# Kernel tuning notes

Hardware: AMD Instinct MI355X
Metric: run time of the kernel (lower is better)

Reference implementation:

```python
import jax, jax.numpy as jnp
import numpy as np

H = 4  # num_heads


def setup_inputs() -> dict:
    key = jax.random.key(0)
    ks = jax.random.split(key, 9)
    B, N, Cin, Chid = 4, 2048, 256, 256
    Cs = Cin // 4
    f = lambda k, shape: jax.random.normal(k, shape, dtype=jnp.float32)
    return {
        "s": f(ks[0], (B, N, Cin)),
        "h": f(ks[1], (B, N, Cs)),
        "sh": f(ks[2], (B, N, Chid)),
        "temperature": jnp.ones((H, 1, 1), jnp.float32) * 0.1,
        "temperature2": jnp.ones((H, 1, 1), jnp.float32) * 0.1,
        "Wq_c": f(ks[3], (Cin, Cin)) * 0.02,
        "Wq_s": f(ks[4], (Chid, Chid)) * 0.02,
        "Wk_c": f(ks[5], (Chid, Chid)) * 0.02,
        "Wv_c": f(ks[6], (Chid, Chid)) * 0.02,
        "Wk_s": f(ks[7], (Chid, Chid)) * 0.02,
        "Wv_s": f(ks[8], (Cs, Cs)) * 0.02,
    }


def reference(s, h, sh, temperature, temperature2, Wq_c, Wq_s, Wk_c, Wv_c, Wk_s, Wv_s):
    B, N, C = sh.shape
    C_c = s.shape[2]
    C_s = h.shape[2]
    d = C // H
    d_c = C_c // H
    d_s = C_s // H

    # projections (Linear without bias: x @ W.T)
    q_c = (s @ Wq_c.T).reshape(B, H, N, d_c).swapaxes(-1, -2)  # (B,H,d_c,N)
    q_s = (sh @ Wq_s.T).reshape(B, H, N, d)
    k_c = (sh @ Wk_c.T).reshape(B, H, N, d)
    v_c = (sh @ Wv_c.T).reshape(B, H, N, d)
    k_s = (sh @ Wk_s.T).reshape(B, H, N, d)
    v_s = (h @ Wv_s.T).reshape(B, H, N, d_s)

    scale = 1.0 / jnp.sqrt(jnp.float32(d))

    # channel branch: (B,H,d_c,N)@(B,H,N,d) -> (B,H,d_c,d)
    attn_ca = jax.nn.softmax((q_c @ k_c) * scale * temperature, axis=-1)
    # dropout is identity at inference
    x_ca = (attn_ca @ v_c.swapaxes(-2, -1)).reshape(B, N, C_c)  # raw reshape, faithful to torch

    # spatial branch: (B,H,N,N)
    attn_sa = jax.nn.softmax(
        jnp.einsum("bhnd,bhmd->bhnm", q_s, k_s) * scale * temperature2, axis=-1
    )
    x_sa = (attn_sa @ v_s).reshape(B, N, C_s)  # raw reshape, faithful to torch

    return jnp.concatenate([x_ca, x_sa], axis=2)  # (B,N,C_c+C_s)
```

## Files before the change

### kernel.cpp

```cpp
#include <hip/hip_runtime.h>
#include <math.h>


constexpr int Bb = 4, Nn = 2048, Hh = 4;
constexpr int PROJ_EL = Nn * 256;
constexpr int HEAD_EL = Nn * 64;

typedef __attribute__((ext_vector_type(8))) short short8_t;
typedef __attribute__((ext_vector_type(4))) float f32x4;

__device__ __forceinline__ ushort f2bf(float x) {
    union { float f; unsigned u; } v; v.f = x;
    unsigned r = v.u + 0x7fffu + ((v.u >> 16) & 1u);
    return (ushort)(r >> 16);
}
__device__ __forceinline__ float bf2f(ushort x) {
    union { unsigned u; float f; } v; v.u = ((unsigned)x) << 16;
    return v.f;
}
__device__ __forceinline__ void gl_lds16(const ushort* g, ushort* l) {
    __builtin_amdgcn_global_load_lds(
        (const __attribute__((address_space(1))) void*)g,
        (__attribute__((address_space(3))) void*)l, 16, 0, 0);
}

constexpr size_t OFF_SB    = 0;
constexpr size_t OFF_SHB   = OFF_SB   + 1024 * 1024;
constexpr size_t OFF_HB    = OFF_SHB  + 1024 * 1024;
constexpr size_t OFF_WQC   = OFF_HB   + 256 * 1024;
constexpr size_t OFF_WCAT  = OFF_WQC  + 32 * 1024;
constexpr size_t OFF_PQC   = OFF_WCAT + 128 * 1024;
constexpr size_t OFF_PQS   = OFF_PQC  + 1024 * 1024;
constexpr size_t OFF_PKC   = OFF_PQS  + 1024 * 1024;
constexpr size_t OFF_PVC   = OFF_PKC  + 1024 * 1024;
constexpr size_t OFF_PKS   = OFF_PVC  + 1024 * 1024;
constexpr size_t OFF_PVST  = OFF_PKS  + 1024 * 1024;
constexpr size_t OFF_PART  = OFF_PVST + 256 * 1024;
constexpr size_t OFF_SCA   = OFF_PART + 512 * 1024;
constexpr size_t OFF_WVS   = OFF_SCA  + 32 * 1024;

constexpr unsigned SEG0 = 2097152;
constexpr unsigned SEG1 = SEG0 + 2097152;
constexpr unsigned SEG2 = SEG1 + 524288;
constexpr unsigned SEG3 = SEG2 + 65536;
constexpr unsigned SEG4 = SEG3 + 65536;
constexpr unsigned SEG5 = SEG4 + 65536;
constexpr unsigned SEG6 = SEG5 + 65536;
constexpr unsigned SEG7 = SEG6 + 65536;
constexpr unsigned SEG8 = SEG7 + 4096;

__global__ __launch_bounds__(256) void convert_all(
    const float* __restrict__ s, const float* __restrict__ sh,
    const float* __restrict__ h, const float* __restrict__ wqc,
    const float* __restrict__ wqs, const float* __restrict__ wkc,
    const float* __restrict__ wvc, const float* __restrict__ wks,
    const float* __restrict__ wvs,
    ushort* __restrict__ sb, ushort* __restrict__ shb, ushort* __restrict__ hb,
    ushort* __restrict__ wqcb, ushort* __restrict__ wcatb, ushort* __restrict__ wvsb)
{
    unsigned e = (blockIdx.x * 256u + threadIdx.x) * 8u;
    if (e >= SEG8) return;
    const float* src; ushort* dst; unsigned off;
    if      (e < SEG0) { src = s;   dst = sb;             off = e; }
    else if (e < SEG1) { src = sh;  dst = shb;            off = e - SEG0; }
    else if (e < SEG2) { src = h;   dst = hb;             off = e - SEG1; }
    else if (e < SEG3) { src = wqc; dst = wqcb;           off = e - SEG2; }
    else if (e < SEG4) { src = wqs; dst = wcatb;          off = e - SEG3; }
    else if (e < SEG5) { src = wkc; dst = wcatb + 65536;  off = e - SEG4; }
    else if (e < SEG6) { src = wvc; dst = wcatb + 131072; off = e - SEG5; }
    else if (e < SEG7) { src = wks; dst = wcatb + 196608; off = e - SEG6; }
    else               { src = wvs; dst = wvsb;           off = e - SEG7; }
    float4 f0 = *(const float4*)&src[off];
    float4 f1 = *(const float4*)&src[off + 4];
    short8_t o;
    o[0] = f2bf(f0.x); o[1] = f2bf(f0.y); o[2] = f2bf(f0.z); o[3] = f2bf(f0.w);
    o[4] = f2bf(f1.x); o[5] = f2bf(f1.y); o[6] = f2bf(f1.z); o[7] = f2bf(f1.w);
    *(short8_t*)&dst[off] = o;
}

__device__ __forceinline__ void gemm_tile_body(
    const ushort* __restrict__ X, const ushort* __restrict__ W,
    ushort* __restrict__ d0, ushort* __restrict__ d1,
    ushort* __restrict__ d2, ushort* __restrict__ d3, int K,
    int m0, int n0, ushort (*Xs)[64], ushort (*Ws)[64])
{
    const int t = threadIdx.x;
    const int w = t >> 6, l = t & 63, c = l & 15, g = l >> 4;
    const int wr = w >> 1, wc = w & 1;
    const int r8 = l >> 3;

    f32x4 acc[4][4] = {};

    for (int k0 = 0; k0 < K; k0 += 64) {
        __syncthreads();
        #pragma unroll
        for (int q = 0; q < 4; ++q) {
            const int rbase = w * 32 + q * 8;
            const int row = rbase + r8;
            const int slot = (l & 7) ^ (row & 7);
            gl_lds16(&X[(size_t)(m0 + row) * K + k0 + slot * 8], &Xs[rbase][0]);
            gl_lds16(&W[(size_t)(n0 + row) * K + k0 + slot * 8], &Ws[rbase][0]);
        }
        __syncthreads();
        #pragma unroll
        for (int ks = 0; ks < 2; ++ks) {
            short8_t af[4], bf[4];
            #pragma unroll
            for (int rt = 0; rt < 4; ++rt) {
                const int R = wr * 64 + rt * 16 + c;
                af[rt] = *(const short8_t*)&Xs[R][(((4 * ks + g) ^ (R & 7)) * 8)];
            }
            #pragma unroll
            for (int ct = 0; ct < 4; ++ct) {
                const int R = wc * 64 + ct * 16 + c;
                bf[ct] = *(const short8_t*)&Ws[R][(((4 * ks + g) ^ (R & 7)) * 8)];
            }
            #pragma unroll
            for (int rt = 0; rt < 4; ++rt)
                #pragma unroll
                for (int ct = 0; ct < 4; ++ct)
                    acc[rt][ct] = __builtin_amdgcn_mfma_f32_16x16x32_bf16(
                        af[rt], bf[ct], acc[rt][ct], 0, 0, 0);
        }
    }

    const int seg = n0 >> 8;
    ushort* dst = seg == 0 ? d0 : seg == 1 ? d1 : seg == 2 ? d2 : d3;
    const int colbase = (n0 & 255) + wc * 64;
    #pragma unroll
    for (int rt = 0; rt < 4; ++rt)
        #pragma unroll
        for (int ct = 0; ct < 4; ++ct)
            #pragma unroll
            for (int r = 0; r < 4; ++r) {
                int mrow = m0 + wr * 64 + rt * 16 + 4 * g + r;
                int col = colbase + ct * 16 + c;
                dst[(size_t)mrow * 256 + col] = f2bf(acc[rt][ct][r]);
            }
}

__device__ __forceinline__ void vs_tile_body(
    const ushort* __restrict__ Wvs, const ushort* __restrict__ Hb,
    ushort* __restrict__ Cvt, int vbid)
{
    const int t = threadIdx.x;
    const int w = t >> 6, l = t & 63, c = l & 15, g = l >> 4;
    const int n0 = vbid * 256 + w * 64;

    f32x4 acc[4][4] = {};
    #pragma unroll
    for (int ks = 0; ks < 2; ++ks) {
        short8_t af[4], bfr[4];
        #pragma unroll
        for (int rt = 0; rt < 4; ++rt)
            af[rt] = *(const short8_t*)&Wvs[(size_t)(rt * 16 + c) * 64 + ks * 32 + 8 * g];
        #pragma unroll
        for (int ct = 0; ct < 4; ++ct)
            bfr[ct] = *(const short8_t*)&Hb[(size_t)(n0 + ct * 16 + c) * 64 + ks * 32 + 8 * g];
        #pragma unroll
        for (int rt = 0; rt < 4; ++rt)
            #pragma unroll
            for (int ct = 0; ct < 4; ++ct)
                acc[rt][ct] = __builtin_amdgcn_mfma_f32_16x16x32_bf16(
                    af[rt], bfr[ct], acc[rt][ct], 0, 0, 0);
    }
    #pragma unroll
    for (int rt = 0; rt < 4; ++rt)
        #pragma unroll
        for (int ct = 0; ct < 4; ++ct)
            #pragma unroll
            for (int r = 0; r < 4; ++r) {
                int cc = rt * 16 + 4 * g + r;
                int m  = n0 + ct * 16 + c;
                int b  = m >> 11, n = m & 2047;
                int L  = n * 64 + cc;
                int hh = L >> 15;
                int k  = (L & 32767) >> 4;
                int d  = L & 15;
                Cvt[(size_t)((b * 4 + hh) * 16 + d) * 2048 + k] = f2bf(acc[rt][ct][r]);
            }
}

__global__ __launch_bounds__(256) void proj_all(
    const ushort* __restrict__ shb, const ushort* __restrict__ wcatb,
    ushort* __restrict__ Pqs, ushort* __restrict__ Pkc,
    ushort* __restrict__ Pvc, ushort* __restrict__ Pks,
    const ushort* __restrict__ sb, const ushort* __restrict__ wqcb,
    ushort* __restrict__ Pqc,
    const ushort* __restrict__ wvsb, const ushort* __restrict__ hb,
    ushort* __restrict__ PvsT)
{
    __shared__ ushort Xs[128][64];
    __shared__ ushort Ws[128][64];
    const int bid = blockIdx.x;
    if (bid < 512) {
        gemm_tile_body(shb, wcatb, Pqs, Pkc, Pvc, Pks, 256,
                       (bid >> 3) * 128, (bid & 7) * 128, Xs, Ws);
    } else if (bid < 640) {
        const int r = bid - 512;
        gemm_tile_body(sb, wqcb, Pqc, Pqc, Pqc, Pqc, 256,
                       (r >> 1) * 128, (r & 1) * 128, Xs, Ws);
    } else {
        vs_tile_body(wvsb, hb, PvsT, bid - 640);
    }
}

__global__ __launch_bounds__(256) void chan_qk_mfma(const ushort* __restrict__ Pqc,
                                                    const ushort* __restrict__ Pkc,
                                                    float* __restrict__ part)
{
    const int ch = blockIdx.x, hh = blockIdx.y, b = blockIdx.z;
    const ushort* Q = Pqc + (size_t)b * PROJ_EL + (size_t)hh * HEAD_EL;
    const ushort* Kk = Pkc + (size_t)b * PROJ_EL + (size_t)hh * HEAD_EL;
    __shared__ ushort Qt[64][72];
    __shared__ ushort Kt[64][72];
    const int t = threadIdx.x;
    const int w = t >> 6, l = t & 63, c = l & 15, g = l >> 4;
    const int srow = t & 63;
    const int scol0 = (t >> 6) * 8;

    f32x4 acc[4] = {};

    for (int sub = 0; sub < 4; ++sub) {
        const int r0 = ch * 256 + sub * 64;
        __syncthreads();
        #pragma unroll
        for (int pass = 0; pass < 2; ++pass) {
            const int cbase = scol0 + pass * 32;
            short8_t qv = *(const short8_t*)&Q[(size_t)(r0 + srow) * 64 + cbase];
            short8_t kv = *(const short8_t*)&Kk[(size_t)(r0 + srow) * 64 + cbase];
            #pragma unroll
            for (int j = 0; j < 8; ++j) {
                Qt[cbase + j][srow] = (ushort)qv[j];
                Kt[cbase + j][srow] = (ushort)kv[j];
            }
        }
        __syncthreads();
        #pragma unroll
        for (int ks = 0; ks < 2; ++ks) {
            short8_t af = *(const short8_t*)&Qt[w * 16 + c][ks * 32 + 8 * g];
            #pragma unroll
            for (int ct = 0; ct < 4; ++ct) {
                short8_t bf = *(const short8_t*)&Kt[ct * 16 + c][ks * 32 + 8 * g];
                acc[ct] = __builtin_amdgcn_mfma_f32_16x16x32_bf16(af, bf, acc[ct], 0, 0, 0);
            }
        }
    }

    float* P = part + (((size_t)(b * 4 + hh) * 8 + ch) << 12);
    #pragma unroll
    for (int ct = 0; ct < 4; ++ct)
        #pragma unroll
        for (int r = 0; r < 4; ++r)
            P[(w * 16 + 4 * g + r) * 64 + ct * 16 + c] = acc[ct][r];
}

__global__ __launch_bounds__(256) void chan_softmax(const float* __restrict__ part,
                                                    const float* __restrict__ temp,
                                                    ushort* __restrict__ Sca)
{
    const int bh = blockIdx.x;
    const int hsel = bh & 3;
    const int t = threadIdx.x;
    const int i = t >> 2, q = t & 3;
    const float sT = 0.125f * temp[hsel];

    float v[16];
    #pragma unroll
    for (int jj = 0; jj < 16; ++jj) v[jj] = 0.f;
    #pragma unroll
    for (int cc = 0; cc < 8; ++cc) {
        const float* p = &part[((size_t)bh * 8 + cc) * 4096 + i * 64 + q * 16];
        #pragma unroll
        for (int j4 = 0; j4 < 4; ++j4) {
            float4 f = *(const float4*)&p[j4 * 4];
            v[j4 * 4 + 0] += f.x; v[j4 * 4 + 1] += f.y;
            v[j4 * 4 + 2] += f.z; v[j4 * 4 + 3] += f.w;
        }
    }
    float m = -1e30f;
    #pragma unroll
    for (int jj = 0; jj < 16; ++jj) { v[jj] *= sT; m = fmaxf(m, v[jj]); }
    m = fmaxf(m, __shfl_xor(m, 1, 4));
    m = fmaxf(m, __shfl_xor(m, 2, 4));
    float sum = 0.f;
    #pragma unroll
    for (int jj = 0; jj < 16; ++jj) { v[jj] = __expf(v[jj] - m); sum += v[jj]; }
    sum += __shfl_xor(sum, 1, 4);
    sum += __shfl_xor(sum, 2, 4);
    const float inv = 1.0f / sum;
    ushort* dst = &Sca[((size_t)bh << 12) + i * 64 + q * 16];
    #pragma unroll
    for (int j4 = 0; j4 < 4; ++j4) {
        ushort4 r;
        r.x = f2bf(v[j4 * 4 + 0] * inv); r.y = f2bf(v[j4 * 4 + 1] * inv);
        r.z = f2bf(v[j4 * 4 + 2] * inv); r.w = f2bf(v[j4 * 4 + 3] * inv);
        *(ushort4*)&dst[j4 * 4] = r;
    }
}

__device__ __forceinline__ void chan_pv_body(
    const ushort* __restrict__ Sca, const ushort* __restrict__ Pvc,
    float* __restrict__ out, int b, int hh, int nc, int wv, int l)
{
    const int c = l & 15, g = l >> 4;
    const ushort* S = Sca + ((size_t)(b * 4 + hh) << 12);
    const ushort* V = Pvc + (size_t)b * PROJ_EL + (size_t)hh * HEAD_EL;
    const int n0w = nc * 256 + wv * 64;

    f32x4 acc[4][4] = {};
    #pragma unroll
    for (int ks = 0; ks < 2; ++ks) {
        short8_t af[4], bfr[4];
        #pragma unroll
        for (int rt = 0; rt < 4; ++rt)
            af[rt] = *(const short8_t*)&S[(size_t)(rt * 16 + c) * 64 + ks * 32 + 8 * g];
        #pragma unroll
        for (int ct = 0; ct < 4; ++ct)
            bfr[ct] = *(const short8_t*)&V[(size_t)(n0w + ct * 16 + c) * 64 + ks * 32 + 8 * g];
        #pragma unroll
        for (int rt = 0; rt < 4; ++rt)
            #pragma unroll
            for (int ct = 0; ct < 4; ++ct)
                acc[rt][ct] = __builtin_amdgcn_mfma_f32_16x16x32_bf16(
                    af[rt], bfr[ct], acc[rt][ct], 0, 0, 0);
    }

    float* ob = out + (size_t)b * (Nn * 320);
    #pragma unroll
    for (int rt = 0; rt < 4; ++rt)
        #pragma unroll
        for (int ct = 0; ct < 4; ++ct)
            #pragma unroll
            for (int r = 0; r < 4; ++r) {
                int i = rt * 16 + 4 * g + r;
                int nn = n0w + ct * 16 + c;
                int rem = hh * 131072 + i * 2048 + nn;
                ob[(rem >> 8) * 320 + (rem & 255)] = acc[rt][ct][r];
            }
}

__global__ __launch_bounds__(512, 2) void spatial_pv(
    const ushort* __restrict__ Pqs, const ushort* __restrict__ Pks,
    const ushort* __restrict__ PvsT, const float* __restrict__ temp2,
    const ushort* __restrict__ Sca, const ushort* __restrict__ Pvc,
    float* __restrict__ out)
{
    if (blockIdx.x < 64) {
        const int task = blockIdx.x * 8 + (threadIdx.x >> 6);
        const int b2 = task >> 7, rem = task & 127;
        const int hh2 = rem >> 5, rem2 = rem & 31;
        const int nc = rem2 >> 2, wv = rem2 & 3;
        chan_pv_body(Sca, Pvc, out, b2, hh2, nc, wv, threadIdx.x & 63);
        return;
    }

    const int i0 = blockIdx.x - 64;
    const int xcd = i0 & 7, j = i0 >> 3;
    const int hsel = xcd + 8 * (j & 1);
    const int qb = j >> 1;
    const int b = hsel >> 2, hh = hsel & 3;

    const int t = threadIdx.x, w = t >> 6, l = t & 63;
    const int c = l & 15, g = l >> 4;
    const int qg = w >> 1, kh = w & 1;

    __shared__ ushort Kbuf[2][2][64][72];
    __shared__ ushort Vbuf[2][2][16][72];
    __shared__ ushort P_lds[8][2][16][72];
    __shared__ float  O_red[8][2][16][16];
    __shared__ float  L_red[8][2][16];

    const ushort* Qh = Pqs + (size_t)b * PROJ_EL + (size_t)hh * HEAD_EL;
    const ushort* Kh = Pks + (size_t)b * PROJ_EL + (size_t)hh * HEAD_EL;
    const ushort* Vt = PvsT + (size_t)((b * 4 + hh) * 16) * 2048;
    const float sT2 = 0.125f * temp2[hh] * 1.44269504f;

    const int q0 = qb * 128 + qg * 32;
    const ushort* qpA = Qh + (size_t)(q0 + c) * 64 + 8 * g;
    const ushort* qpB = qpA + 16 * 64;
    const short8_t qfA0 = *(const short8_t*)qpA;
    const short8_t qfA1 = *(const short8_t*)(qpA + 32);
    const short8_t qfB0 = *(const short8_t*)qpB;
    const short8_t qfB1 = *(const short8_t*)(qpB + 32);

    f32x4 oaccA = {0.f, 0.f, 0.f, 0.f}, oaccB = {0.f, 0.f, 0.f, 0.f};
    float lsumA = 0.f, lsumB = 0.f;
    ushort* PwA = &P_lds[w][0][0][0];
    ushort* PwB = &P_lds[w][1][0][0];

    const int sh_ = t >> 8, th = t & 255;
    const int krow = th >> 2, ksub = (th & 3) * 16;
    const int vrow = th >> 4, vcol = (th & 15) * 4;

    {
        const int kb = (sh_ * 16) * 64;
        short8_t k0 = *(const short8_t*)&Kh[(size_t)(kb + krow) * 64 + ksub];
        short8_t k1 = *(const short8_t*)&Kh[(size_t)(kb + krow) * 64 + ksub + 8];
        uint2 v0 = *(const uint2*)&Vt[(size_t)vrow * 2048 + kb + vcol];
        *(short8_t*)&Kbuf[sh_][0][krow][ksub]     = k0;
        *(short8_t*)&Kbuf[sh_][0][krow][ksub + 8] = k1;
        *(uint2*)&Vbuf[sh_][0][vrow][vcol] = v0;
    }

    short8_t kreg0, kreg1; uint2 vreg;
    for (int it = 0; it < 16; ++it) {
        const int cur = it & 1;

        if (it < 15) {
            const int nb = (sh_ * 16 + it + 1) * 64;
            kreg0 = *(const short8_t*)&Kh[(size_t)(nb + krow) * 64 + ksub];
            kreg1 = *(const short8_t*)&Kh[(size_t)(nb + krow) * 64 + ksub + 8];
            vreg = *(const uint2*)&Vt[(size_t)vrow * 2048 + nb + vcol];
        }

        __syncthreads();

        #pragma unroll
        for (int tc = 0; tc < 4; ++tc) {
            short8_t kf0 = *(const short8_t*)&Kbuf[kh][cur][tc * 16 + c][8 * g];
            short8_t kf1 = *(const short8_t*)&Kbuf[kh][cur][tc * 16 + c][32 + 8 * g];
            f32x4 z = {0.f, 0.f, 0.f, 0.f};
            f32x4 sa = __builtin_amdgcn_mfma_f32_16x16x32_bf16(kf0, qfA0, z, 0, 0, 0);
            sa = __builtin_amdgcn_mfma_f32_16x16x32_bf16(kf1, qfA1, sa, 0, 0, 0);
            f32x4 sb2 = __builtin_amdgcn_mfma_f32_16x16x32_bf16(kf0, qfB0, z, 0, 0, 0);
            sb2 = __builtin_amdgcn_mfma_f32_16x16x32_bf16(kf1, qfB1, sb2, 0, 0, 0);

            float a0 = __builtin_amdgcn_exp2f(sa[0] * sT2);
            float a1 = __builtin_amdgcn_exp2f(sa[1] * sT2);
            float a2 = __builtin_amdgcn_exp2f(sa[2] * sT2);
            float a3 = __builtin_amdgcn_exp2f(sa[3] * sT2);
            lsumA += (a0 + a1) + (a2 + a3);
            unsigned ua, ub;
            asm("v_cvt_pk_bf16_f32 %0, %1, %2" : "=v"(ua) : "v"(a0), "v"(a1));
            asm("v_cvt_pk_bf16_f32 %0, %1, %2" : "=v"(ub) : "v"(a2), "v"(a3));
            *(unsigned*)&PwA[(size_t)c * 72 + tc * 16 + 4 * g]     = ua;
            *(unsigned*)&PwA[(size_t)c * 72 + tc * 16 + 4 * g + 2] = ub;

            float b0 = __builtin_amdgcn_exp2f(sb2[0] * sT2);
            float b1 = __builtin_amdgcn_exp2f(sb2[1] * sT2);
            float b2 = __builtin_amdgcn_exp2f(sb2[2] * sT2);
            float b3 = __builtin_amdgcn_exp2f(sb2[3] * sT2);
            lsumB += (b0 + b1) + (b2 + b3);
            unsigned vb0, vb1;
            asm("v_cvt_pk_bf16_f32 %0, %1, %2" : "=v"(vb0) : "v"(b0), "v"(b1));
            asm("v_cvt_pk_bf16_f32 %0, %1, %2" : "=v"(vb1) : "v"(b2), "v"(b3));
            *(unsigned*)&PwB[(size_t)c * 72 + tc * 16 + 4 * g]     = vb0;
            *(unsigned*)&PwB[(size_t)c * 72 + tc * 16 + 4 * g + 2] = vb1;
        }
        __builtin_amdgcn_sched_barrier(0);
        #pragma unroll
        for (int ks = 0; ks < 2; ++ks) {
            short8_t vf = *(const short8_t*)&Vbuf[kh][cur][c][ks * 32 + 8 * g];
            short8_t pfA = *(const short8_t*)&PwA[(size_t)c * 72 + ks * 32 + 8 * g];
            oaccA = __builtin_amdgcn_mfma_f32_16x16x32_bf16(vf, pfA, oaccA, 0, 0, 0);
            short8_t pfB = *(const short8_t*)&PwB[(size_t)c * 72 + ks * 32 + 8 * g];
            oaccB = __builtin_amdgcn_mfma_f32_16x16x32_bf16(vf, pfB, oaccB, 0, 0, 0);
        }

        if (it < 15) {
            *(short8_t*)&Kbuf[sh_][cur ^ 1][krow][ksub]     = kreg0;
            *(short8_t*)&Kbuf[sh_][cur ^ 1][krow][ksub + 8] = kreg1;
            *(uint2*)&Vbuf[sh_][cur ^ 1][vrow][vcol] = vreg;
        }
    }

    lsumA += __shfl_xor(lsumA, 16);
    lsumA += __shfl_xor(lsumA, 32);
    lsumB += __shfl_xor(lsumB, 16);
    lsumB += __shfl_xor(lsumB, 32);

    *(float4*)&O_red[w][0][c][4 * g] = make_float4(oaccA[0], oaccA[1], oaccA[2], oaccA[3]);
    *(float4*)&O_red[w][1][c][4 * g] = make_float4(oaccB[0], oaccB[1], oaccB[2], oaccB[3]);
    if (g == 0) { L_red[w][0][c] = lsumA; L_red[w][1][c] = lsumB; }
    __syncthreads();

    if (kh == 0) {
        #pragma unroll
        for (int ss = 0; ss < 2; ++ss) {
            float4 o0 = *(const float4*)&O_red[w][ss][c][4 * g];
            float4 o1 = *(const float4*)&O_red[w + 1][ss][c][4 * g];
            float ltot = L_red[w][ss][c] + L_red[w + 1][ss][c];
            const float inv = 1.0f / ltot;
            const int nn = q0 + ss * 16 + c;
            const int n = hh * 512 + (nn >> 2);
            const int cc = 256 + ((nn & 3) << 4) + 4 * g;
            float4 o4 = make_float4((o0.x + o1.x) * inv, (o0.y + o1.y) * inv,
                                    (o0.z + o1.z) * inv, (o0.w + o1.w) * inv);
            *(float4*)&out[((size_t)b * Nn + n) * 320 + cc] = o4;
        }
    }
}

extern "C" void kernel_launch(void* const* d_in, const int* in_sizes, int n_in,
                              void* d_out, int out_size, void* d_ws, size_t ws_size,
                              hipStream_t stream)
{
    const float* s     = (const float*)d_in[0];
    const float* h     = (const float*)d_in[1];
    const float* sh    = (const float*)d_in[2];
    const float* temp  = (const float*)d_in[3];
    const float* temp2 = (const float*)d_in[4];
    const float* Wq_c  = (const float*)d_in[5];
    const float* Wq_s  = (const float*)d_in[6];
    const float* Wk_c  = (const float*)d_in[7];
    const float* Wv_c  = (const float*)d_in[8];
    const float* Wk_s  = (const float*)d_in[9];
    const float* Wv_s  = (const float*)d_in[10];
    float* out = (float*)d_out;
    float* ws = (float*)d_ws;

    ushort* sb    = (ushort*)(ws + OFF_SB);
    ushort* shb   = (ushort*)(ws + OFF_SHB);
    ushort* hb    = (ushort*)(ws + OFF_HB);
    ushort* wqcb  = (ushort*)(ws + OFF_WQC);
    ushort* wcatb = (ushort*)(ws + OFF_WCAT);
    ushort* wvsb  = (ushort*)(ws + OFF_WVS);
    ushort* Pqc   = (ushort*)(ws + OFF_PQC);
    ushort* Pqs   = (ushort*)(ws + OFF_PQS);
    ushort* Pkc   = (ushort*)(ws + OFF_PKC);
    ushort* Pvc   = (ushort*)(ws + OFF_PVC);
    ushort* Pks   = (ushort*)(ws + OFF_PKS);
    ushort* PvsT  = (ushort*)(ws + OFF_PVST);
    float*  part  = ws + OFF_PART;
    ushort* Sca   = (ushort*)(ws + OFF_SCA);

    const dim3 blk(256);

    convert_all<<<dim3((SEG8 / 8 + 255) / 256), blk, 0, stream>>>(
        s, sh, h, Wq_c, Wq_s, Wk_c, Wv_c, Wk_s, Wv_s,
        sb, shb, hb, wqcb, wcatb, wvsb);

    proj_all<<<dim3(672), blk, 0, stream>>>(
        shb, wcatb, Pqs, Pkc, Pvc, Pks, sb, wqcb, Pqc, wvsb, hb, PvsT);

    chan_qk_mfma<<<dim3(8, 4, 4), blk, 0, stream>>>(Pqc, Pkc, part);
    chan_softmax<<<dim3(16), blk, 0, stream>>>(part, temp, Sca);

    spatial_pv<<<dim3(320), dim3(512), 0, stream>>>(
        Pqs, Pks, PvsT, temp2, Sca, Pvc, out);
}
```

Before: 59.66 us.

## Stream K/V tiles straight to LDS with global_load_lds and XOR swizzle

Replaces the register-staged K/V prefetch (global load into registers, then an LDS store after compute) with direct global-to-LDS async loads. The loads are issued right after the barrier into the other buffer. Padded rows are swapped for an XOR-swizzled 64-wide layout to avoid bank conflicts, and the P stores are merged into single 64-bit writes. This cuts VGPR pressure and LDS store instructions in the spatial attention loop. In exchange it depends on the barrier ordering being correct for the async LDS writes, since no explicit vmcnt wait is visible before the next iteration's reads.

```diff
diff --git a/kernel.cpp b/kernel.cpp
--- a/kernel.cpp
+++ b/kernel.cpp
@@ -365,8 +365,8 @@
     const int c = l & 15, g = l >> 4;
     const int qg = w >> 1, kh = w & 1;
 
-    __shared__ ushort Kbuf[2][2][64][72];
-    __shared__ ushort Vbuf[2][2][16][72];
+    __shared__ ushort Kbuf[2][2][64][64];
+    __shared__ ushort Vbuf[2][2][16][64];
     __shared__ ushort P_lds[8][2][16][72];
     __shared__ float  O_red[8][2][16][16];
     __shared__ float  L_red[8][2][16];
@@ -389,37 +389,55 @@
     ushort* PwA = &P_lds[w][0][0][0];
     ushort* PwB = &P_lds[w][1][0][0];
 
-    const int sh_ = t >> 8, th = t & 255;
-    const int krow = th >> 2, ksub = (th & 3) * 16;
-    const int vrow = th >> 4, vcol = (th & 15) * 4;
+    const int sh_ = t >> 8, wvh = w & 3;
+    const int r8 = l >> 3;
 
     {
         const int kb = (sh_ * 16) * 64;
-        short8_t k0 = *(const short8_t*)&Kh[(size_t)(kb + krow) * 64 + ksub];
-        short8_t k1 = *(const short8_t*)&Kh[(size_t)(kb + krow) * 64 + ksub + 8];
-        uint2 v0 = *(const uint2*)&Vt[(size_t)vrow * 2048 + kb + vcol];
-        *(short8_t*)&Kbuf[sh_][0][krow][ksub]     = k0;
-        *(short8_t*)&Kbuf[sh_][0][krow][ksub + 8] = k1;
-        *(uint2*)&Vbuf[sh_][0][vrow][vcol] = v0;
-    }
-
-    short8_t kreg0, kreg1; uint2 vreg;
+        #pragma unroll
+        for (int q2 = 0; q2 < 2; ++q2) {
+            const int rbase = wvh * 16 + q2 * 8;
+            const int row = rbase + r8;
+            const int slot = (l & 7) ^ (row & 7);
+            gl_lds16(&Kh[(size_t)(kb + row) * 64 + slot * 8], &Kbuf[sh_][0][rbase][0]);
+        }
+        if (wvh < 2) {
+            const int rbase = wvh * 8;
+            const int row = rbase + r8;
+            const int slot = (l & 7) ^ (row & 7);
+            gl_lds16(&Vt[(size_t)row * 2048 + kb + slot * 8], &Vbuf[sh_][0][rbase][0]);
+        }
+    }
+
     for (int it = 0; it < 16; ++it) {
         const int cur = it & 1;
 
+        __syncthreads();
+
         if (it < 15) {
             const int nb = (sh_ * 16 + it + 1) * 64;
-            kreg0 = *(const short8_t*)&Kh[(size_t)(nb + krow) * 64 + ksub];
-            kreg1 = *(const short8_t*)&Kh[(size_t)(nb + krow) * 64 + ksub + 8];
-            vreg = *(const uint2*)&Vt[(size_t)vrow * 2048 + nb + vcol];
-        }
-
-        __syncthreads();
-
+            #pragma unroll
+            for (int q2 = 0; q2 < 2; ++q2) {
+                const int rbase = wvh * 16 + q2 * 8;
+                const int row = rbase + r8;
+                const int slot = (l & 7) ^ (row & 7);
+                gl_lds16(&Kh[(size_t)(nb + row) * 64 + slot * 8],
+                         &Kbuf[sh_][cur ^ 1][rbase][0]);
+            }
+            if (wvh < 2) {
+                const int rbase = wvh * 8;
+                const int row = rbase + r8;
+                const int slot = (l & 7) ^ (row & 7);
+                gl_lds16(&Vt[(size_t)row * 2048 + nb + slot * 8],
+                         &Vbuf[sh_][cur ^ 1][rbase][0]);
+            }
+        }
+
+        const int rswz = c & 7;
         #pragma unroll
         for (int tc = 0; tc < 4; ++tc) {
-            short8_t kf0 = *(const short8_t*)&Kbuf[kh][cur][tc * 16 + c][8 * g];
-            short8_t kf1 = *(const short8_t*)&Kbuf[kh][cur][tc * 16 + c][32 + 8 * g];
+            short8_t kf0 = *(const short8_t*)&Kbuf[kh][cur][tc * 16 + c][(g ^ rswz) * 8];
+            short8_t kf1 = *(const short8_t*)&Kbuf[kh][cur][tc * 16 + c][((4 + g) ^ rswz) * 8];
             f32x4 z = {0.f, 0.f, 0.f, 0.f};
             f32x4 sa = __builtin_amdgcn_mfma_f32_16x16x32_bf16(kf0, qfA0, z, 0, 0, 0);
             sa = __builtin_amdgcn_mfma_f32_16x16x32_bf16(kf1, qfA1, sa, 0, 0, 0);
@@ -431,37 +449,29 @@
             float a2 = __builtin_amdgcn_exp2f(sa[2] * sT2);
             float a3 = __builtin_amdgcn_exp2f(sa[3] * sT2);
             lsumA += (a0 + a1) + (a2 + a3);
-            unsigned ua, ub;
-            asm("v_cvt_pk_bf16_f32 %0, %1, %2" : "=v"(ua) : "v"(a0), "v"(a1));
-            asm("v_cvt_pk_bf16_f32 %0, %1, %2" : "=v"(ub) : "v"(a2), "v"(a3));
-            *(unsigned*)&PwA[(size_t)c * 72 + tc * 16 + 4 * g]     = ua;
-            *(unsigned*)&PwA[(size_t)c * 72 + tc * 16 + 4 * g + 2] = ub;
+            uint2 pkA;
+            asm("v_cvt_pk_bf16_f32 %0, %1, %2" : "=v"(pkA.x) : "v"(a0), "v"(a1));
+            asm("v_cvt_pk_bf16_f32 %0, %1, %2" : "=v"(pkA.y) : "v"(a2), "v"(a3));
+            *(uint2*)&PwA[(size_t)c * 72 + tc * 16 + 4 * g] = pkA;
 
             float b0 = __builtin_amdgcn_exp2f(sb2[0] * sT2);
             float b1 = __builtin_amdgcn_exp2f(sb2[1] * sT2);
             float b2 = __builtin_amdgcn_exp2f(sb2[2] * sT2);
             float b3 = __builtin_amdgcn_exp2f(sb2[3] * sT2);
             lsumB += (b0 + b1) + (b2 + b3);
-            unsigned vb0, vb1;
-            asm("v_cvt_pk_bf16_f32 %0, %1, %2" : "=v"(vb0) : "v"(b0), "v"(b1));
-            asm("v_cvt_pk_bf16_f32 %0, %1, %2" : "=v"(vb1) : "v"(b2), "v"(b3));
-            *(unsigned*)&PwB[(size_t)c * 72 + tc * 16 + 4 * g]     = vb0;
-            *(unsigned*)&PwB[(size_t)c * 72 + tc * 16 + 4 * g + 2] = vb1;
+            uint2 pkB;
+            asm("v_cvt_pk_bf16_f32 %0, %1, %2" : "=v"(pkB.x) : "v"(b0), "v"(b1));
+            asm("v_cvt_pk_bf16_f32 %0, %1, %2" : "=v"(pkB.y) : "v"(b2), "v"(b3));
+            *(uint2*)&PwB[(size_t)c * 72 + tc * 16 + 4 * g] = pkB;
         }
         __builtin_amdgcn_sched_barrier(0);
         #pragma unroll
         for (int ks = 0; ks < 2; ++ks) {
-            short8_t vf = *(const short8_t*)&Vbuf[kh][cur][c][ks * 32 + 8 * g];
+            short8_t vf = *(const short8_t*)&Vbuf[kh][cur][c][((4 * ks + g) ^ (c & 7)) * 8];
             short8_t pfA = *(const short8_t*)&PwA[(size_t)c * 72 + ks * 32 + 8 * g];
             oaccA = __builtin_amdgcn_mfma_f32_16x16x32_bf16(vf, pfA, oaccA, 0, 0, 0);
             short8_t pfB = *(const short8_t*)&PwB[(size_t)c * 72 + ks * 32 + 8 * g];
             oaccB = __builtin_amdgcn_mfma_f32_16x16x32_bf16(vf, pfB, oaccB, 0, 0, 0);
-        }
-
-        if (it < 15) {
-            *(short8_t*)&Kbuf[sh_][cur ^ 1][krow][ksub]     = kreg0;
-            *(short8_t*)&Kbuf[sh_][cur ^ 1][krow][ksub + 8] = kreg1;
-            *(uint2*)&Vbuf[sh_][cur ^ 1][vrow][vcol] = vreg;
         }
     }
 
```

Measured after the change: 60.95 us. +2.1%, slower.
